# Optimization experiments

Hardware: AMD Instinct MI355X
Metric: run time of the kernel (lower is better)

The kernel has to match this reference:

```python
import jax, jax.numpy as jnp
import numpy as np

B, S, H = 2, 2048, 768
NH, HD = 12, 64
I = 1152
EPS = 1e-5
ROPE_BASE = 10000.0
MAX_POS = 8192


def _layernorm(x, w, b):
    mu = jnp.mean(x, axis=-1, keepdims=True)
    var = jnp.mean(jnp.square(x - mu), axis=-1, keepdims=True)
    return (x - mu) / jnp.sqrt(var + EPS) * w + b


def _rope_tables():
    pos = jnp.arange(MAX_POS, dtype=jnp.float32)
    theta = 1.0 / (ROPE_BASE ** (jnp.arange(0, HD, 2, dtype=jnp.float32) / HD))
    ang = pos[:, None] * theta  # [MAX_POS, HD//2]
    return jnp.cos(ang), jnp.sin(ang)


def _apply_rope(x, cos, sin):
    # x: [B, NH, S, HD]; cos/sin: [B, 1, S, HD//2]; interleaved pair rotation
    x2 = x.reshape(*x.shape[:-1], HD // 2, 2)
    x0, x1 = x2[..., 0], x2[..., 1]
    rot = jnp.stack([x0 * cos - x1 * sin, x1 * cos + x0 * sin], axis=-1)
    return rot.reshape(x.shape)


def setup_inputs() -> dict:
    key = jax.random.key(0)
    ks = jax.random.split(key, 8)
    std = 0.02
    return {
        "hidden_states": jax.random.normal(ks[0], (B, S, H), dtype=jnp.float32),
        "attention_mask": jnp.zeros((B, 1, S, S), dtype=jnp.float32),
        "sliding_window_mask": jnp.zeros((B, 1, S, S), dtype=jnp.float32),
        "position_ids": jnp.tile(jnp.arange(S, dtype=jnp.int32)[None, :], (B, 1)),
        "qkv_w": jax.random.normal(ks[1], (3 * H, H), dtype=jnp.float32) * std,
        "o_w": jax.random.normal(ks[2], (H, H), dtype=jnp.float32) * std,
        "attn_norm_w": jnp.ones((H,), dtype=jnp.float32),
        "attn_norm_b": jnp.zeros((H,), dtype=jnp.float32),
        "mlp_norm_w": jnp.ones((H,), dtype=jnp.float32),
        "mlp_norm_b": jnp.zeros((H,), dtype=jnp.float32),
        "wi_w": jax.random.normal(ks[3], (2 * I, H), dtype=jnp.float32) * std,
        "wi_b": jnp.zeros((2 * I,), dtype=jnp.float32),
        "wo_w": jax.random.normal(ks[4], (H, I), dtype=jnp.float32) * std,
        "wo_b": jnp.zeros((H,), dtype=jnp.float32),
    }


def reference(hidden_states, attention_mask, sliding_window_mask, position_ids,
              qkv_w, o_w, attn_norm_w, attn_norm_b, mlp_norm_w, mlp_norm_b,
              wi_w, wi_b, wo_w, wo_b):
    # --- attention block (layer_id != 0 -> pre-LN) ---
    x = _layernorm(hidden_states, attn_norm_w, attn_norm_b)
    qkv = jnp.einsum('bsh,oh->bso', x, qkv_w)          # [B,S,3H] (no bias)
    qkv = qkv.reshape(B, S, 3, NH, HD)
    qkv = jnp.transpose(qkv, (0, 3, 2, 1, 4))          # [B,NH,3,S,HD]
    q, k, v = qkv[:, :, 0], qkv[:, :, 1], qkv[:, :, 2]

    cos_t, sin_t = _rope_tables()
    cos = cos_t[position_ids][:, None]                 # [B,1,S,HD//2]
    sin = sin_t[position_ids][:, None]
    q = _apply_rope(q, cos, sin)
    k = _apply_rope(k, cos, sin)

    scale = HD ** -0.5
    scores = jnp.einsum('bhqd,bhkd->bhqk', q, k) * scale
    scores = scores + attention_mask + sliding_window_mask
    probs = jax.nn.softmax(scores, axis=-1)
    ctx = jnp.einsum('bhqk,bhkd->bhqd', probs, v)      # [B,NH,S,HD]
    ctx = jnp.transpose(ctx, (0, 2, 1, 3)).reshape(B, S, H)
    attn_out = jnp.einsum('bsh,oh->bso', ctx, o_w)
    hidden = hidden_states + attn_out

    # --- GeGLU MLP block ---
    y = _layernorm(hidden, mlp_norm_w, mlp_norm_b)
    h = jax.nn.gelu(jnp.einsum('bsh,oh->bso', y, wi_w) + wi_b, approximate=False)
    gated = h[..., 0::2] * h[..., 1::2]                # strided gelu-gate split
    mlp_out = jnp.einsum('bsi,oi->bso', gated, wo_w) + wo_b
    return hidden + mlp_out
```

## Files before the change

kernel.cpp:

```cpp
#include <hip/hip_runtime.h>
#include <hip/hip_bf16.h>
#include <math.h>

#define B_  2
#define S_  2048
#define H_  768
#define NH_ 12
#define HD_ 64
#define I_  1152
#define LOG2E 1.4426950408889634f
#define SCALE_L2E 0.18033688011112042f

typedef __bf16 bf16;
typedef __bf16 bf16x8 __attribute__((ext_vector_type(8)));
typedef float  f32x4  __attribute__((ext_vector_type(4)));
typedef float  f32x16 __attribute__((ext_vector_type(16)));
typedef float  f32x2  __attribute__((ext_vector_type(2)));
typedef unsigned u32x2 __attribute__((ext_vector_type(2)));
typedef unsigned u32x4 __attribute__((ext_vector_type(4)));

__device__ __forceinline__ void gll16(const void* g, void* l) {
  __builtin_amdgcn_global_load_lds((const __attribute__((address_space(1))) void*)g,
                                   (__attribute__((address_space(3))) void*)l, 16, 0, 0);
}

__device__ __forceinline__ unsigned pack_bf16(float a, float b) {
  union { bf16 e[2]; unsigned u; } r;
  r.e[0] = (bf16)a; r.e[1] = (bf16)b;
  return r.u;
}

__device__ __forceinline__ void plswap(unsigned &a, unsigned &b) {
  asm volatile("v_permlane32_swap_b32 %0, %1" : "+v"(a), "+v"(b));
}
__device__ __forceinline__ float halfmax(float x) {
  unsigned a = __builtin_bit_cast(unsigned, x), b = a;
  plswap(a, b);
  return fmaxf(__builtin_bit_cast(float, a), __builtin_bit_cast(float, b));
}

#define CN1 442368
#define CN2 147456
#define CN3 442368
#define CN4 221184
__global__ void cvt_all(const float* __restrict__ s0, const float* __restrict__ s1,
                        const float* __restrict__ s2, const float* __restrict__ s3,
                        bf16* __restrict__ d0, bf16* __restrict__ d1,
                        bf16* __restrict__ d2, bf16* __restrict__ d3) {
  int i = blockIdx.x * 256 + threadIdx.x;
  const float* s; bf16* d; int o;
  if (i < CN1)            { s = s0; d = d0; o = i; }
  else if (i < CN1 + CN2) { s = s1; d = d1; o = i - CN1; }
  else if (i < CN1 + CN2 + CN3) { s = s2; d = d2; o = i - CN1 - CN2; }
  else                    { s = s3; d = d3; o = i - CN1 - CN2 - CN3; }
  float4 v = ((const float4*)s)[o];
  union { bf16 e[4]; uint2 u; } r;
  r.e[0] = (bf16)v.x; r.e[1] = (bf16)v.y; r.e[2] = (bf16)v.z; r.e[3] = (bf16)v.w;
  ((uint2*)d)[o] = r.u;
}

__global__ void build_rope_tbl(f32x2* __restrict__ tbl) {
  int i = blockIdx.x * 256 + threadIdx.x;
  int jp = i & 31, pos = i >> 5;
  float th = exp2f((float)jp * (-13.287712379549449f / 32.f));
  float sn, cs;
  sincosf((float)pos * th, &sn, &cs);
  tbl[i] = (f32x2){cs, sn};
}

__global__ __launch_bounds__(256) void combine_mask2(const float* __restrict__ a,
                                                     const float* __restrict__ b,
                                                     bf16* __restrict__ E,
                                                     unsigned* __restrict__ flags) {
  const int kt = blockIdx.x, qi = blockIdx.y, bb = blockIdx.z, tid = threadIdx.x;
  float sm[8][4];
  bool ok = true;
#pragma unroll
  for (int c = 0; c < 8; ++c) {
    int idx4 = c * 256 + tid;
    int r = idx4 >> 4, col = (idx4 & 15) * 4;
    size_t g = ((size_t)(bb * S_) + qi * 128 + r) * S_ + kt * 64 + col;
    float4 x = *(const float4*)(a + g);
    float4 y = *(const float4*)(b + g);
    sm[c][0] = x.x + y.x; sm[c][1] = x.y + y.y;
    sm[c][2] = x.z + y.z; sm[c][3] = x.w + y.w;
    ok = ok && (sm[c][0] == 0.f) && (sm[c][1] == 0.f) && (sm[c][2] == 0.f) && (sm[c][3] == 0.f);
  }
  __shared__ unsigned sh[4];
  unsigned long long bal = __ballot(ok);
  if ((tid & 63) == 0) sh[tid >> 6] = (bal == ~0ull) ? 1u : 0u;
  __syncthreads();
  unsigned flag = sh[0] & sh[1] & sh[2] & sh[3];
  if (tid == 0) flags[(bb * 16 + qi) * 32 + kt] = flag;
  if (!flag) {
#pragma unroll
    for (int c = 0; c < 8; ++c) {
      int idx4 = c * 256 + tid;
      int r = idx4 >> 4, col = (idx4 & 15) * 4;
      size_t g = ((size_t)(bb * S_) + qi * 128 + r) * S_ + kt * 64 + col;
      union { bf16 e[4]; uint2 u; } w;
      w.e[0] = (bf16)__expf(sm[c][0]); w.e[1] = (bf16)__expf(sm[c][1]);
      w.e[2] = (bf16)__expf(sm[c][2]); w.e[3] = (bf16)__expf(sm[c][3]);
      *(uint2*)(E + g) = w.u;
    }
  }
}

__global__ __launch_bounds__(256) void ln_bf16(const float* __restrict__ in,
                                               const float* __restrict__ w,
                                               const float* __restrict__ bia,
                                               bf16* __restrict__ out) {
  int row = blockIdx.x, tid = threadIdx.x;
  const float* x = in + (size_t)row * H_;
  float v0 = x[tid], v1 = x[tid + 256], v2 = x[tid + 512];
  float s = v0 + v1 + v2;
  float q = v0 * v0 + v1 * v1 + v2 * v2;
  for (int o = 1; o < 64; o <<= 1) { s += __shfl_xor(s, o); q += __shfl_xor(q, o); }
  __shared__ float rs[4], rq[4];
  if ((tid & 63) == 0) { rs[tid >> 6] = s; rq[tid >> 6] = q; }
  __syncthreads();
  s = rs[0] + rs[1] + rs[2] + rs[3];
  q = rq[0] + rq[1] + rq[2] + rq[3];
  float mu = s * (1.f / H_);
  float var = q * (1.f / H_) - mu * mu;
  float rstd = rsqrtf(var + 1e-5f);
  bf16* orow = out + (size_t)row * H_;
  orow[tid]       = (bf16)((v0 - mu) * rstd * w[tid]       + bia[tid]);
  orow[tid + 256] = (bf16)((v1 - mu) * rstd * w[tid + 256] + bia[tid + 256]);
  orow[tid + 512] = (bf16)((v2 - mu) * rstd * w[tid + 512] + bia[tid + 512]);
}

__device__ __forceinline__ void gemm_main_loop(
    int K, const bf16* __restrict__ aSrc0, const bf16* __restrict__ aSrc1,
    const bf16* __restrict__ bSrc0, const bf16* __restrict__ bSrc1,
    bf16* As, bf16* Bs, int tid, int wr, int wc, int l15, int lg,
    f32x4 (&acc)[4][4]) {
  const int NT = K >> 5;
  auto stage = [&](int t, int buf) {
    const int ko = t * 32;
    bf16* ad = As + buf * 4096 + tid * 8;
    bf16* bd = Bs + buf * 4096 + tid * 8;
    gll16(aSrc0 + ko, ad);
    gll16(aSrc1 + ko, ad + 2048);
    gll16(bSrc0 + ko, bd);
    gll16(bSrc1 + ko, bd + 2048);
  };
  stage(0, 0);
  __syncthreads();
  for (int t = 0; t < NT; ++t) {
    const int cur = t & 1;
    if (t + 1 < NT) stage(t + 1, cur ^ 1);
    const bf16* Ab = As + cur * 4096;
    const bf16* Bb = Bs + cur * 4096;
    bf16x8 af[4], bfr[4];
#pragma unroll
    for (int i = 0; i < 4; ++i)
      af[i] = *(const bf16x8*)&Ab[(wr + i * 16 + l15) * 32 + lg * 8];
#pragma unroll
    for (int j = 0; j < 4; ++j)
      bfr[j] = *(const bf16x8*)&Bb[(wc + j * 16 + l15) * 32 + lg * 8];
    __builtin_amdgcn_s_setprio(1);
#pragma unroll
    for (int i = 0; i < 4; ++i)
#pragma unroll
      for (int j = 0; j < 4; ++j)
        acc[i][j] = __builtin_amdgcn_mfma_f32_16x16x32_bf16(af[i], bfr[j], acc[i][j], 0, 0, 0);
    __builtin_amdgcn_s_setprio(0);
    __syncthreads();
  }
}

template<bool BIAS, bool RES>
__global__ __launch_bounds__(256) void gemm64d(const bf16* __restrict__ A,
                                               const bf16* __restrict__ W,
                                               float* __restrict__ C,
                                               const float* __restrict__ bias,
                                               const float* __restrict__ res,
                                               int M, int N, int K) {
  __shared__ bf16 As[2 * 64 * 32];
  __shared__ bf16 Bs[2 * 128 * 32];
  const int tid = threadIdx.x, lane = tid & 63, wv = tid >> 6;
  const int bm = blockIdx.y * 64, bn = blockIdx.x * 128;
  const int wr = (wv >> 1) * 32, wc = (wv & 1) * 64;
  const int l15 = lane & 15, lg = lane >> 4;

  f32x4 acc[2][4] = {};
  const int srow = tid >> 2, scc = (tid & 3) * 8;
  const bf16* aSrc0 = A + (size_t)(bm + srow) * K + scc;
  const bf16* bSrc0 = W + (size_t)(bn + srow) * K + scc;
  const bf16* bSrc1 = W + (size_t)(bn + 64 + srow) * K + scc;

  const int NT = K >> 5;
  auto stage = [&](int t, int buf) {
    const int ko = t * 32;
    gll16(aSrc0 + ko, As + buf * 2048 + tid * 8);
    gll16(bSrc0 + ko, Bs + buf * 4096 + tid * 8);
    gll16(bSrc1 + ko, Bs + buf * 4096 + 2048 + tid * 8);
  };
  stage(0, 0);
  __syncthreads();
  for (int t = 0; t < NT; ++t) {
    const int cur = t & 1;
    if (t + 1 < NT) stage(t + 1, cur ^ 1);
    const bf16* Ab = As + cur * 2048;
    const bf16* Bb = Bs + cur * 4096;
    bf16x8 af[2], bfr[4];
#pragma unroll
    for (int i = 0; i < 2; ++i)
      af[i] = *(const bf16x8*)&Ab[(wr + i * 16 + l15) * 32 + lg * 8];
#pragma unroll
    for (int j = 0; j < 4; ++j)
      bfr[j] = *(const bf16x8*)&Bb[(wc + j * 16 + l15) * 32 + lg * 8];
    __builtin_amdgcn_s_setprio(1);
#pragma unroll
    for (int i = 0; i < 2; ++i)
#pragma unroll
      for (int j = 0; j < 4; ++j)
        acc[i][j] = __builtin_amdgcn_mfma_f32_16x16x32_bf16(af[i], bfr[j], acc[i][j], 0, 0, 0);
    __builtin_amdgcn_s_setprio(0);
    __syncthreads();
  }

  const int r0 = lg * 4;
#pragma unroll
  for (int i = 0; i < 2; ++i) {
#pragma unroll
    for (int j = 0; j < 4; ++j) {
      int col = bn + wc + j * 16 + l15;
      float bv = BIAS ? bias[col] : 0.f;
#pragma unroll
      for (int r = 0; r < 4; ++r) {
        int row = bm + wr + i * 16 + r0 + r;
        float v = acc[i][j][r] + bv;
        if (RES) v += res[(size_t)row * N + col];
        C[(size_t)row * N + col] = v;
      }
    }
  }
}

__global__ __launch_bounds__(256) void gemm_qkv(const bf16* __restrict__ A,
                                                const bf16* __restrict__ W,
                                                const int* __restrict__ pid,
                                                const f32x2* __restrict__ tbl,
                                                bf16* __restrict__ qb,
                                                bf16* __restrict__ kb,
                                                bf16* __restrict__ vb) {
  __shared__ bf16 As[2 * 128 * 32];
  __shared__ bf16 Bs[2 * 128 * 32];
  const int tid = threadIdx.x, lane = tid & 63, wv = tid >> 6;
  const int bm = blockIdx.y * 128, bn = blockIdx.x * 128;
  const int wr = (wv >> 1) * 64, wc = (wv & 1) * 64;
  const int l15 = lane & 15, lg = lane >> 4;
  const int K = H_;

  f32x4 acc[4][4] = {};
  const int srow = tid >> 2, scc = (tid & 3) * 8;
  gemm_main_loop(K,
      A + (size_t)(bm + srow) * K + scc, A + (size_t)(bm + 64 + srow) * K + scc,
      W + (size_t)(bn + srow) * K + scc, W + (size_t)(bn + 64 + srow) * K + scc,
      As, Bs, tid, wr, wc, l15, lg, acc);

  const int r0 = lg * 4;
  const int sect = bn / H_;
  const int hcb = (bn % H_) + wc;
  bf16* dst0 = sect == 0 ? qb : (sect == 1 ? kb : vb);
#pragma unroll
  for (int i = 0; i < 4; ++i) {
#pragma unroll
    for (int r = 0; r < 4; ++r) {
      const int row = bm + wr + i * 16 + r0 + r;
      const int b = row >> 11, s = row & 2047;
      const int pos = (sect < 2) ? pid[row] : 0;
#pragma unroll
      for (int j = 0; j < 4; ++j) {
        const int hc = hcb + j * 16 + l15;
        const int h = hc >> 6, d = hc & 63;
        float x = acc[i][j][r];
        float v;
        if (sect < 2) {
          f32x2 cs = tbl[pos * 32 + (d >> 1)];
          float xp = __shfl_xor(x, 1);
          v = (d & 1) ? fmaf(x, cs.x, xp * cs.y) : fmaf(x, cs.x, -xp * cs.y);
        } else {
          v = x;
        }
        float vp = __shfl_xor(v, 1);
        if (!(l15 & 1))
          *(unsigned*)(dst0 + ((size_t)(b * NH_ + h) * S_ + s) * HD_ + d) = pack_bf16(v, vp);
      }
    }
  }
}

__global__ __launch_bounds__(256) void gemm_wi(const bf16* __restrict__ A,
                                               const bf16* __restrict__ W,
                                               const float* __restrict__ bias,
                                               bf16* __restrict__ g) {
  __shared__ bf16 As[2 * 128 * 32];
  __shared__ bf16 Bs[2 * 128 * 32];
  const int tid = threadIdx.x, lane = tid & 63, wv = tid >> 6;
  const int bm = blockIdx.y * 128, bn = blockIdx.x * 128;
  const int wr = (wv >> 1) * 64, wc = (wv & 1) * 64;
  const int l15 = lane & 15, lg = lane >> 4;
  const int K = H_;

  f32x4 acc[4][4] = {};
  const int srow = tid >> 2, scc = (tid & 3) * 8;
  gemm_main_loop(K,
      A + (size_t)(bm + srow) * K + scc, A + (size_t)(bm + 64 + srow) * K + scc,
      W + (size_t)(bn + srow) * K + scc, W + (size_t)(bn + 64 + srow) * K + scc,
      As, Bs, tid, wr, wc, l15, lg, acc);

  const int r0 = lg * 4;
#pragma unroll
  for (int j = 0; j < 4; ++j) {
    const int col = bn + wc + j * 16 + l15;
    const float bv = bias[col];
#pragma unroll
    for (int i = 0; i < 4; ++i) {
#pragma unroll
      for (int r = 0; r < 4; ++r) {
        const int row = bm + wr + i * 16 + r0 + r;
        float x = acc[i][j][r] + bv;
        float gx = 0.5f * x * (1.f + erff(x * 0.70710678118654752f));
        float gp = __shfl_xor(gx, 1);
        if (!(l15 & 1))
          g[(size_t)row * I_ + (col >> 1)] = (bf16)(gx * gp);
      }
    }
  }
}

__global__ __launch_bounds__(512, 4) void attn8(
    const bf16* __restrict__ Q, const bf16* __restrict__ Kg, const bf16* __restrict__ Vg,
    const bf16* __restrict__ Eg, const unsigned* __restrict__ flags, bf16* __restrict__ ctx) {
  __shared__ bf16 Kt[2][2][64 * 64];
  __shared__ bf16 Vt[2][2][64 * 64];
  const int tid = threadIdx.x, lane = tid & 63, wv = tid >> 6;
  const int wq = wv & 3, ks = wv >> 2;
  const int qi = blockIdx.x, h = blockIdx.y, b = blockIdx.z;
  const int l31 = lane & 31, hi = lane >> 5, b4 = (lane >> 4) & 1;
  const size_t headbase = (size_t)(b * NH_ + h) * S_ * HD_;
  const bf16* kbase = Kg + headbase;
  const bf16* vbase = Vg + headbase;
  const unsigned* fptr = flags + (b * 16 + qi) * 32;
  const int kswz = (l31 & 7) << 4;
  const int qrow = qi * 128 + wq * 32 + l31;
  const bf16* Erow = Eg + (size_t)b * S_ * S_ + (size_t)qrow * S_;

  union { unsigned u[4]; bf16x8 v; } ones;
  ones.u[0] = ones.u[1] = ones.u[2] = ones.u[3] = 0x3F803F80u;

  bf16x8 qf[4];
  {
    const bf16* qp = Q + headbase + (size_t)qrow * HD_;
#pragma unroll
    for (int kc = 0; kc < 4; ++kc)
      qf[kc] = *(const bf16x8*)(qp + kc * 16 + hi * 8);
  }

  auto stageK = [&](int t, int bs, int par) {
    int kr = tid >> 3, sl = tid & 7;
    gll16(kbase + (size_t)t * 64 * HD_ + kr * HD_ + (sl ^ (kr & 7)) * 8, &Kt[bs][par][tid * 8]);
  };
  auto stageV = [&](int t, int bs, int par) {
    int p = tid >> 7, kr = (tid & 127) >> 1, hf = tid & 1;
    gll16(vbase + (size_t)t * 64 * HD_ + kr * HD_ + (p >> 1) * 32 + (p & 1) * 16 + hf * 8,
          &Vt[bs][par][tid * 8]);
  };

  float m = -1e30f, l = 0.f;
  f32x16 oa[2] = {};

  stageK(0, 0, 0); stageV(0, 0, 0);
  stageK(1, 0, 1); stageV(1, 0, 1);
  unsigned fl = fptr[ks];
  __syncthreads();

  for (int r = 0; r < 16; ++r) {
    const int cur = r & 1;
    const int kt = 2 * r + ks;
    unsigned flN = 1;
    if (r < 15) {
      flN = fptr[kt + 2];
      stageK(2 * r + 2, cur ^ 1, 0); stageV(2 * r + 2, cur ^ 1, 0);
      stageK(2 * r + 3, cur ^ 1, 1); stageV(2 * r + 3, cur ^ 1, 1);
    }

    f32x16 sv[2];
    __builtin_amdgcn_s_setprio(1);
#pragma unroll
    for (int kb = 0; kb < 2; ++kb) {
      f32x16 s = {};
#pragma unroll
      for (int kc = 0; kc < 4; ++kc) {
        const bf16x8 kf = *(const bf16x8*)((const char*)&Kt[cur][ks][0] +
            ((kb * 32 + l31) * 128 + ((kc * 32 + hi * 16) ^ kswz)));
        s = __builtin_amdgcn_mfma_f32_32x32x16_bf16(kf, qf[kc], s, 0, 0, 0);
      }
      sv[kb] = s;
    }
    __builtin_amdgcn_s_setprio(0);

    float p0 = fmaxf(sv[0][0], sv[1][0]), p1 = fmaxf(sv[0][1], sv[1][1]);
    float p2 = fmaxf(sv[0][2], sv[1][2]), p3 = fmaxf(sv[0][3], sv[1][3]);
#pragma unroll
    for (int r2 = 4; r2 < 16; r2 += 4) {
      p0 = fmaxf(p0, fmaxf(sv[0][r2],     sv[1][r2]));
      p1 = fmaxf(p1, fmaxf(sv[0][r2 + 1], sv[1][r2 + 1]));
      p2 = fmaxf(p2, fmaxf(sv[0][r2 + 2], sv[1][r2 + 2]));
      p3 = fmaxf(p3, fmaxf(sv[0][r2 + 3], sv[1][r2 + 3]));
    }
    float pmS = halfmax(fmaxf(fmaxf(p0, p1), fmaxf(p2, p3))) * SCALE_L2E;
    if (__any(pmS - m > 8.f)) {
      float mn = fmaxf(m, pmS);
      float alpha = exp2f(m - mn);
      m = mn;
      l *= alpha;
#pragma unroll
      for (int db = 0; db < 2; ++db)
#pragma unroll
        for (int r2 = 0; r2 < 16; ++r2) oa[db][r2] *= alpha;
    }
#pragma unroll
    for (int kb = 0; kb < 2; ++kb)
#pragma unroll
      for (int r2 = 0; r2 < 16; ++r2)
        sv[kb][r2] = exp2f(fmaf(sv[kb][r2], SCALE_L2E, -m));
    if (!fl) {
#pragma unroll
      for (int kb = 0; kb < 2; ++kb)
#pragma unroll
        for (int rq = 0; rq < 4; ++rq) {
          union { bf16 e[4]; u32x2 u; } eu;
          eu.u = *(const u32x2*)(Erow + (size_t)kt * 64 + kb * 32 + rq * 8 + hi * 4);
#pragma unroll
          for (int j = 0; j < 4; ++j)
            sv[kb][rq * 4 + j] *= (float)eu.e[j];
        }
    }

    unsigned pk[2][4][2];
#pragma unroll
    for (int kb = 0; kb < 2; ++kb)
#pragma unroll
      for (int rq = 0; rq < 4; ++rq)
#pragma unroll
        for (int dd = 0; dd < 2; ++dd)
          pk[kb][rq][dd] = pack_bf16(sv[kb][rq * 4 + dd * 2], sv[kb][rq * 4 + dd * 2 + 1]);
    union { u32x4 u; bf16x8 v; } pauv[4];
#pragma unroll
    for (int kc = 0; kc < 4; ++kc) {
      const int kb = kc >> 1, rb = (kc & 1) * 2;
      unsigned pa0[2], pa1[2];
#pragma unroll
      for (int dd = 0; dd < 2; ++dd) {
        unsigned A = pk[kb][rb][dd], Bv = pk[kb][rb + 1][dd];
        plswap(A, Bv);
        pa0[dd] = A; pa1[dd] = Bv;
      }
      pauv[kc].u = (u32x4){pa0[0], pa0[1], pa1[0], pa1[1]};
    }

    {
      f32x16 ls = {};
#pragma unroll
      for (int kc = 0; kc < 4; ++kc)
        ls = __builtin_amdgcn_mfma_f32_32x32x16_bf16(ones.v, pauv[kc].v, ls, 0, 0, 0);
      l += ls[0];
    }

    const unsigned vlds = (unsigned)(size_t)&Vt[cur][ks][0] + b4 * 1920;
#pragma unroll
    for (int db = 0; db < 2; ++db) {
      u32x2 tr[4][2];
#pragma unroll
      for (int kc = 0; kc < 4; ++kc)
#pragma unroll
        for (int rd = 0; rd < 2; ++rd) {
          unsigned ad = vlds + (db * 4096 + kc * 512 + rd * 128);
          asm volatile("ds_read_b64_tr_b16 %0, %1 offset:0" : "=v"(tr[kc][rd]) : "v"(ad));
        }
      asm volatile("s_waitcnt lgkmcnt(0)" ::: "memory");
      __builtin_amdgcn_sched_barrier(0);
      __builtin_amdgcn_s_setprio(1);
#pragma unroll
      for (int kc = 0; kc < 4; ++kc) {
        union { u32x4 u; bf16x8 v; } vfu;
        vfu.u = (u32x4){tr[kc][0][0], tr[kc][0][1], tr[kc][1][0], tr[kc][1][1]};
        oa[db] = __builtin_amdgcn_mfma_f32_32x32x16_bf16(vfu.v, pauv[kc].v, oa[db], 0, 0, 0);
      }
      __builtin_amdgcn_s_setprio(0);
    }
    __syncthreads();
    fl = flN;
  }

  float* KO = (float*)&Kt[0][0][0];
  float* ML = (float*)&Vt[1][0][0];
  if (ks == 1) {
#pragma unroll
    for (int db = 0; db < 2; ++db)
#pragma unroll
      for (int rq = 0; rq < 4; ++rq) {
        int q4 = (db * 4 + rq) ^ (l31 & 7);
        *(f32x4*)&KO[wq * 2048 + l31 * 64 + hi * 32 + q4 * 4] =
            (f32x4){oa[db][rq * 4], oa[db][rq * 4 + 1], oa[db][rq * 4 + 2], oa[db][rq * 4 + 3]};
      }
    if (hi == 0) { ML[wq * 64 + l31 * 2] = m; ML[wq * 64 + l31 * 2 + 1] = l; }
  }
  __syncthreads();
  if (ks == 0) {
    float m1 = ML[wq * 64 + l31 * 2], l1 = ML[wq * 64 + l31 * 2 + 1];
    float ms = fmaxf(m, m1);
    float a0 = exp2f(m - ms), a1 = exp2f(m1 - ms);
    float inv = 1.f / (l * a0 + l1 * a1);
    a0 *= inv; a1 *= inv;
    char* TR = (char*)&Vt[0][0][0];
#pragma unroll
    for (int db = 0; db < 2; ++db)
#pragma unroll
      for (int rq = 0; rq < 4; ++rq) {
        int q4 = (db * 4 + rq) ^ (l31 & 7);
        f32x4 o1 = *(const f32x4*)&KO[wq * 2048 + l31 * 64 + hi * 32 + q4 * 4];
        float f0 = oa[db][rq * 4 + 0] * a0 + o1[0] * a1;
        float f1 = oa[db][rq * 4 + 1] * a0 + o1[1] * a1;
        float f2 = oa[db][rq * 4 + 2] * a0 + o1[2] * a1;
        float f3 = oa[db][rq * 4 + 3] * a0 + o1[3] * a1;
        u32x2 w = (u32x2){pack_bf16(f0, f1), pack_bf16(f2, f3)};
        *(u32x2*)(TR + wq * 4096 + l31 * 128 + ((db * 64 + rq * 16 + hi * 8) ^ kswz)) = w;
      }
  }
  __syncthreads();
#pragma unroll
  for (int c = 0; c < 2; ++c) {
    int ch = c * 512 + tid, q = ch >> 3, sl = ch & 7;
    u32x4 vv = *(const u32x4*)((const char*)&Vt[0][0][0] +
        ((q >> 5) * 4096 + (q & 31) * 128 + ((sl ^ (q & 7)) * 16)));
    *(u32x4*)(ctx + ((size_t)(b * S_) + qi * 128 + q) * H_ + h * HD_ + sl * 8) = vv;
  }
}

extern "C" void kernel_launch(void* const* d_in, const int* in_sizes, int n_in,
                              void* d_out, int out_size, void* d_ws, size_t ws_size,
                              hipStream_t stream) {
  const float* hs   = (const float*)d_in[0];
  const float* am   = (const float*)d_in[1];
  const float* swm  = (const float*)d_in[2];
  const int*   pid  = (const int*)d_in[3];
  const float* qkvw = (const float*)d_in[4];
  const float* ow   = (const float*)d_in[5];
  const float* anw  = (const float*)d_in[6];
  const float* anb  = (const float*)d_in[7];
  const float* mnw  = (const float*)d_in[8];
  const float* mnb  = (const float*)d_in[9];
  const float* wiw  = (const float*)d_in[10];
  const float* wib  = (const float*)d_in[11];
  const float* wow  = (const float*)d_in[12];
  const float* wob  = (const float*)d_in[13];
  float* out = (float*)d_out;

  char* ws = (char*)d_ws;
  size_t off = 0;
  auto alloc = [&](size_t bytes) { void* p = ws + off; off += (bytes + 255) & ~255ull; return p; };

  bf16* wqkv_b = (bf16*)alloc((size_t)3 * H_ * H_ * 2);
  bf16* wo_b   = (bf16*)alloc((size_t)H_ * H_ * 2);
  bf16* wwi_b  = (bf16*)alloc((size_t)2 * I_ * H_ * 2);
  bf16* wwo_b  = (bf16*)alloc((size_t)H_ * I_ * 2);
  bf16* xln    = (bf16*)alloc((size_t)B_ * S_ * H_ * 2);
  bf16* qb     = (bf16*)alloc((size_t)B_ * NH_ * S_ * HD_ * 2);
  bf16* kb     = (bf16*)alloc((size_t)B_ * NH_ * S_ * HD_ * 2);
  bf16* vb     = (bf16*)alloc((size_t)B_ * NH_ * S_ * HD_ * 2);
  bf16* Eg     = (bf16*)alloc((size_t)B_ * S_ * S_ * 2);
  unsigned* flg= (unsigned*)alloc((size_t)B_ * 16 * 32 * 4);
  bf16* ctx    = (bf16*)alloc((size_t)B_ * S_ * H_ * 2);
  float* hid2  = (float*)alloc((size_t)B_ * S_ * H_ * 4);
  bf16* gated  = (bf16*)alloc((size_t)B_ * S_ * I_ * 2);
  f32x2* tbl   = (f32x2*)alloc((size_t)8192 * 32 * 8);
  (void)ws_size; (void)n_in; (void)in_sizes; (void)out_size;

  const int rows = B_ * S_;

  cvt_all<<<(CN1 + CN2 + CN3 + CN4) / 256, 256, 0, stream>>>(
      qkvw, ow, wiw, wow, wqkv_b, wo_b, wwi_b, wwo_b);
  build_rope_tbl<<<8192 * 32 / 256, 256, 0, stream>>>(tbl);
  combine_mask2<<<dim3(32, 16, B_), 256, 0, stream>>>(am, swm, Eg, flg);

  ln_bf16<<<rows, 256, 0, stream>>>(hs, anw, anb, xln);
  gemm_qkv<<<dim3(3 * H_ / 128, rows / 128), 256, 0, stream>>>(
      xln, wqkv_b, pid, tbl, qb, kb, vb);
  attn8<<<dim3(S_ / 128, NH_, B_), 512, 0, stream>>>(qb, kb, vb, Eg, flg, ctx);
  gemm64d<false, true><<<dim3(H_ / 128, rows / 64), 256, 0, stream>>>(
      ctx, wo_b, hid2, nullptr, hs, rows, H_, H_);
  ln_bf16<<<rows, 256, 0, stream>>>(hid2, mnw, mnb, xln);
  gemm_wi<<<dim3(2 * I_ / 128, rows / 128), 256, 0, stream>>>(xln, wwi_b, wib, gated);
  gemm64d<true, true><<<dim3(H_ / 128, rows / 64), 256, 0, stream>>>(
      gated, wwo_b, out, wob, hid2, rows, H_, I_);
}
```

Baseline: 218.7 us.

## Shrink attention blocks to 64 query rows with single-buffered K tiles

The attention kernel moves from 512-thread blocks covering 128 query rows to 256-thread blocks covering 64 rows, doubling the grid. K tiles become single-buffered: staging of the next K/V tiles now starts after QK^T plus an extra block barrier instead of before it, which cuts shared memory to allow more resident blocks. The output staging buffer is relocated, and the QKV epilogue writes individual bf16 elements instead of shuffling pairs into packed 32-bit stores. The trade-off is less prefetch overlap for K, more total K/V traffic across blocks, and narrower scattered stores in the QKV GEMM.

Result: faster. 205.2 us (-6.1%).

```diff
diff --git a/kernel.cpp b/kernel.cpp
--- a/kernel.cpp
+++ b/kernel.cpp
@@ -285,9 +285,7 @@
         } else {
           v = x;
         }
-        float vp = __shfl_xor(v, 1);
-        if (!(l15 & 1))
-          *(unsigned*)(dst0 + ((size_t)(b * NH_ + h) * S_ + s) * HD_ + d) = pack_bf16(v, vp);
+        dst0[((size_t)(b * NH_ + h) * S_ + s) * HD_ + d] = (bf16)v;
       }
     }
   }
@@ -332,21 +330,21 @@
   }
 }
 
-__global__ __launch_bounds__(512, 4) void attn8(
+__global__ __launch_bounds__(256, 3) void attn4L(
     const bf16* __restrict__ Q, const bf16* __restrict__ Kg, const bf16* __restrict__ Vg,
     const bf16* __restrict__ Eg, const unsigned* __restrict__ flags, bf16* __restrict__ ctx) {
-  __shared__ bf16 Kt[2][2][64 * 64];
+  __shared__ bf16 Ks[2][64 * 64];
   __shared__ bf16 Vt[2][2][64 * 64];
   const int tid = threadIdx.x, lane = tid & 63, wv = tid >> 6;
-  const int wq = wv & 3, ks = wv >> 2;
+  const int wq = wv & 1, ks = wv >> 1;
   const int qi = blockIdx.x, h = blockIdx.y, b = blockIdx.z;
   const int l31 = lane & 31, hi = lane >> 5, b4 = (lane >> 4) & 1;
   const size_t headbase = (size_t)(b * NH_ + h) * S_ * HD_;
   const bf16* kbase = Kg + headbase;
   const bf16* vbase = Vg + headbase;
-  const unsigned* fptr = flags + (b * 16 + qi) * 32;
+  const unsigned* fptr = flags + (b * 16 + (qi >> 1)) * 32;
   const int kswz = (l31 & 7) << 4;
-  const int qrow = qi * 128 + wq * 32 + l31;
+  const int qrow = qi * 64 + wq * 32 + l31;
   const bf16* Erow = Eg + (size_t)b * S_ * S_ + (size_t)qrow * S_;
 
   union { unsigned u[4]; bf16x8 v; } ones;
@@ -360,33 +358,34 @@
       qf[kc] = *(const bf16x8*)(qp + kc * 16 + hi * 8);
   }
 
-  auto stageK = [&](int t, int bs, int par) {
-    int kr = tid >> 3, sl = tid & 7;
-    gll16(kbase + (size_t)t * 64 * HD_ + kr * HD_ + (sl ^ (kr & 7)) * 8, &Kt[bs][par][tid * 8]);
+  auto stageK = [&](int t, int par) {
+#pragma unroll
+    for (int c = 0; c < 2; ++c) {
+      int ch = c * 256 + tid, kr = ch >> 3, sl = ch & 7;
+      gll16(kbase + (size_t)t * 64 * HD_ + kr * HD_ + (sl ^ (kr & 7)) * 8, &Ks[par][ch * 8]);
+    }
   };
   auto stageV = [&](int t, int bs, int par) {
-    int p = tid >> 7, kr = (tid & 127) >> 1, hf = tid & 1;
-    gll16(vbase + (size_t)t * 64 * HD_ + kr * HD_ + (p >> 1) * 32 + (p & 1) * 16 + hf * 8,
-          &Vt[bs][par][tid * 8]);
+#pragma unroll
+    for (int c = 0; c < 2; ++c) {
+      int ch = c * 256 + tid;
+      int p = ch >> 7, kr = (ch & 127) >> 1, hf = ch & 1;
+      gll16(vbase + (size_t)t * 64 * HD_ + kr * HD_ + (p >> 1) * 32 + (p & 1) * 16 + hf * 8,
+            &Vt[bs][par][ch * 8]);
+    }
   };
 
   float m = -1e30f, l = 0.f;
   f32x16 oa[2] = {};
 
-  stageK(0, 0, 0); stageV(0, 0, 0);
-  stageK(1, 0, 1); stageV(1, 0, 1);
+  stageK(0, 0); stageK(1, 1);
+  stageV(0, 0, 0); stageV(1, 0, 1);
   unsigned fl = fptr[ks];
   __syncthreads();
 
-  for (int r = 0; r < 16; ++r) {
-    const int cur = r & 1;
-    const int kt = 2 * r + ks;
-    unsigned flN = 1;
-    if (r < 15) {
-      flN = fptr[kt + 2];
-      stageK(2 * r + 2, cur ^ 1, 0); stageV(2 * r + 2, cur ^ 1, 0);
-      stageK(2 * r + 3, cur ^ 1, 1); stageV(2 * r + 3, cur ^ 1, 1);
-    }
+  for (int R = 0; R < 16; ++R) {
+    const int cur = R & 1;
+    const int kt = 2 * R + ks;
 
     f32x16 sv[2];
     __builtin_amdgcn_s_setprio(1);
@@ -395,13 +394,22 @@
       f32x16 s = {};
 #pragma unroll
       for (int kc = 0; kc < 4; ++kc) {
-        const bf16x8 kf = *(const bf16x8*)((const char*)&Kt[cur][ks][0] +
+        const bf16x8 kf = *(const bf16x8*)((const char*)&Ks[ks][0] +
             ((kb * 32 + l31) * 128 + ((kc * 32 + hi * 16) ^ kswz)));
         s = __builtin_amdgcn_mfma_f32_32x32x16_bf16(kf, qf[kc], s, 0, 0, 0);
       }
       sv[kb] = s;
     }
     __builtin_amdgcn_s_setprio(0);
+
+    __syncthreads();
+
+    unsigned flN = 1;
+    if (R < 15) {
+      flN = fptr[kt + 2];
+      stageK(2 * R + 2, 0); stageK(2 * R + 3, 1);
+      stageV(2 * R + 2, cur ^ 1, 0); stageV(2 * R + 3, cur ^ 1, 1);
+    }
 
     float p0 = fmaxf(sv[0][0], sv[1][0]), p1 = fmaxf(sv[0][1], sv[1][1]);
     float p2 = fmaxf(sv[0][2], sv[1][2]), p3 = fmaxf(sv[0][3], sv[1][3]);
@@ -497,8 +505,9 @@
     fl = flN;
   }
 
-  float* KO = (float*)&Kt[0][0][0];
+  float* KO = (float*)&Ks[0][0];
   float* ML = (float*)&Vt[1][0][0];
+  char*  TR = (char*)&Vt[1][0][0] + 512;
   if (ks == 1) {
 #pragma unroll
     for (int db = 0; db < 2; ++db)
@@ -517,7 +526,6 @@
     float a0 = exp2f(m - ms), a1 = exp2f(m1 - ms);
     float inv = 1.f / (l * a0 + l1 * a1);
     a0 *= inv; a1 *= inv;
-    char* TR = (char*)&Vt[0][0][0];
 #pragma unroll
     for (int db = 0; db < 2; ++db)
 #pragma unroll
@@ -535,10 +543,9 @@
   __syncthreads();
 #pragma unroll
   for (int c = 0; c < 2; ++c) {
-    int ch = c * 512 + tid, q = ch >> 3, sl = ch & 7;
-    u32x4 vv = *(const u32x4*)((const char*)&Vt[0][0][0] +
-        ((q >> 5) * 4096 + (q & 31) * 128 + ((sl ^ (q & 7)) * 16)));
-    *(u32x4*)(ctx + ((size_t)(b * S_) + qi * 128 + q) * H_ + h * HD_ + sl * 8) = vv;
+    int ch = c * 256 + tid, q = ch >> 3, sl = ch & 7;
+    u32x4 vv = *(const u32x4*)(TR + ((q >> 5) * 4096 + (q & 31) * 128 + ((sl ^ (q & 7)) * 16)));
+    *(u32x4*)(ctx + ((size_t)(b * S_) + qi * 64 + q) * H_ + h * HD_ + sl * 8) = vv;
   }
 }
 
@@ -591,7 +598,7 @@
   ln_bf16<<<rows, 256, 0, stream>>>(hs, anw, anb, xln);
   gemm_qkv<<<dim3(3 * H_ / 128, rows / 128), 256, 0, stream>>>(
       xln, wqkv_b, pid, tbl, qb, kb, vb);
-  attn8<<<dim3(S_ / 128, NH_, B_), 512, 0, stream>>>(qb, kb, vb, Eg, flg, ctx);
+  attn4L<<<dim3(S_ / 64, NH_, B_), 256, 0, stream>>>(qb, kb, vb, Eg, flg, ctx);
   gemm64d<false, true><<<dim3(H_ / 128, rows / 64), 256, 0, stream>>>(
       ctx, wo_b, hid2, nullptr, hs, rows, H_, H_);
   ln_bf16<<<rows, 256, 0, stream>>>(hid2, mnw, mnb, xln);
```
